# Performance work log

Hardware: AMD Instinct MI355X
Metric: run time of the kernel (lower is better)

## Reference

```python
import jax, jax.numpy as jnp
import numpy as np

B, N, D_VIS, D_LBL = 64, 256, 2048, 512
H, F_OUT = 8, 256            # n_heads, gat_out_per_head_dim
D_IN = D_VIS + D_LBL         # 2560, GAT input dim
D_GAT = H * F_OUT            # 2048, concat-heads output dim
D_EMB = 512                  # final_embedding_dim
ALPHA = 0.2                  # LeakyReLU negative slope


def setup_inputs() -> dict:
    key = jax.random.key(0)
    ks = jax.random.split(key, 9)
    visual_features = jax.random.normal(ks[0], (B, D_VIS), jnp.float32)
    labels_features = jax.random.normal(ks[1], (N, D_LBL), jnp.float32)
    adj = (jax.random.uniform(ks[2], (N, N)) < 0.1).astype(jnp.float32)
    label_adj_matrix = jnp.maximum(adj, jnp.eye(N, dtype=jnp.float32))
    s = 1.0 / np.sqrt(D_IN)
    W_gat = jax.random.uniform(ks[3], (D_IN, H, F_OUT), jnp.float32, -s, s)
    a_src = jax.random.uniform(ks[4], (H, F_OUT), jnp.float32, -s, s)
    a_dst = jax.random.uniform(ks[5], (H, F_OUT), jnp.float32, -s, s)
    sg = 1.0 / np.sqrt(D_GAT)
    pool_q = jax.random.uniform(ks[6], (D_GAT,), jnp.float32, -sg, sg)
    fc_W = jax.random.uniform(ks[7], (D_GAT, D_EMB), jnp.float32, -sg, sg)
    fc_b = jax.random.uniform(ks[8], (D_EMB,), jnp.float32, -sg, sg)
    return {"visual_features": visual_features, "labels_features": labels_features,
            "label_adj_matrix": label_adj_matrix, "W_gat": W_gat, "a_src": a_src,
            "a_dst": a_dst, "pool_q": pool_q, "fc_W": fc_W, "fc_b": fc_b}


def reference(visual_features, labels_features, label_adj_matrix,
              W_gat, a_src, a_dst, pool_q, fc_W, fc_b):
    # Build per-sample contextualized label node features: (B, N, D_IN)
    x = jnp.concatenate(
        [jnp.broadcast_to(labels_features[None], (B, N, D_LBL)),
         jnp.broadcast_to(visual_features[:, None, :], (B, N, D_VIS))], axis=-1)
    # Multi-head GAT layer, batched over B (the torch code loops over B)
    Wh = jnp.einsum('bnd,dhf->bnhf', x, W_gat)            # (B, N, H, F)
    src = jnp.einsum('bnhf,hf->bhn', Wh, a_src)           # (B, H, N)
    dst = jnp.einsum('bnhf,hf->bhn', Wh, a_dst)           # (B, H, N)
    e = src[:, :, :, None] + dst[:, :, None, :]           # (B, H, N, N)
    e = jnp.where(e > 0, e, ALPHA * e)                    # LeakyReLU
    mask = (label_adj_matrix > 0)[None, None]             # (1, 1, N, N)
    scores = jnp.where(mask, e, jnp.float32(-9e15))
    attn = jax.nn.softmax(scores, axis=-1)                # (B, H, N, N)
    out = jnp.einsum('bhij,bjhf->bihf', attn, Wh)         # (B, N, H, F)
    out = jax.nn.elu(out.reshape(B, N, D_GAT))            # concat heads + ELU
    # attention pooling over label nodes
    pw = jax.nn.softmax(jnp.einsum('bnd,d->bn', out, pool_q), axis=-1)
    pooled = jnp.einsum('bn,bnd->bd', pw, out)            # (B, D_GAT)
    return pooled @ fc_W + fc_b                           # (B, D_EMB)
```

## Files before the change

### kernel.cpp

```cpp
#include <hip/hip_runtime.h>
#include <hip/hip_bf16.h>
#include <math.h>

#define BB 64
#define NN 256
#define D_VIS 2048
#define D_LBL 512
#define HH 8
#define FF 256
#define DG 2048
#define DE 512
#define ALPHA 0.2f
#define PSTRIDE 264

using bf16 = __hip_bfloat16;
using short8 = __attribute__((ext_vector_type(8))) short;
using f32x4  = __attribute__((ext_vector_type(4))) float;
__device__ __forceinline__ float b2f(bf16 x) { return __bfloat162float(x); }
__device__ __forceinline__ unsigned short f2bs(float x) {
    bf16 h = __float2bfloat16(x);
    unsigned short u;
    __builtin_memcpy(&u, &h, 2);
    return u;
}

__global__ void __launch_bounds__(256) k_wh(const float* __restrict__ labels,
                                            const float* __restrict__ visual,
                                            const float* __restrict__ Wg,
                                            unsigned short* __restrict__ WhLbT,
                                            float* __restrict__ WhVz,
                                            const float* __restrict__ aSrc,
                                            const float* __restrict__ aDst,
                                            float* __restrict__ srcLp,
                                            float* __restrict__ dstLp,
                                            float* __restrict__ srcVp,
                                            float* __restrict__ dstVp) {
    __shared__ unsigned short As[32][72];
    __shared__ unsigned short Bs[64][72];
    const int t = threadIdx.x;
    const int w = t >> 6;
    const int lane = t & 63;
    const int l15 = lane & 15, quad = lane >> 4;
    const int n0 = blockIdx.x * 64;
    const int p2 = blockIdx.x & 3;
    const int y = blockIdx.y;
    const bool isL = (y < 8);
    const int q = y - 8;
    const int m0  = isL ? y * 32 : (q & 1) * 32;
    const int z   = isL ? 0 : (q >> 1);
    const int kb0 = z * 512;
    const float* A = isL ? labels : visual;
    const int lda  = isL ? D_LBL : D_VIS;
    const float* Wb = Wg + (isL ? 0 : (size_t)D_LBL * DG);

    f32x4 acc[2];
    acc[0] = (f32x4){0.f, 0.f, 0.f, 0.f};
    acc[1] = (f32x4){0.f, 0.f, 0.f, 0.f};

    for (int kc = 0; kc < 8; ++kc) {
        const int kb = kb0 + kc * 64;
#pragma unroll
        for (int p = 0; p < 2; ++p) {
            const int idx = t + 256 * p;
            const int r = idx >> 4, q4 = idx & 15;
            const float4 v = *(const float4*)(A + (size_t)(m0 + r) * lda + kb + 4 * q4);
            unsigned short s4[4] = {f2bs(v.x), f2bs(v.y), f2bs(v.z), f2bs(v.w)};
            __builtin_memcpy(&As[r][4 * q4], s4, 8);
        }
#pragma unroll
        for (int p = 0; p < 4; ++p) {
            const int kk = (t >> 4) + 16 * p;
            const int c4 = (t & 15) * 4;
            const float4 v = *(const float4*)(Wb + (size_t)(kb + kk) * DG + n0 + c4);
            Bs[c4 + 0][kk] = f2bs(v.x);
            Bs[c4 + 1][kk] = f2bs(v.y);
            Bs[c4 + 2][kk] = f2bs(v.z);
            Bs[c4 + 3][kk] = f2bs(v.w);
        }
        __syncthreads();
#pragma unroll
        for (int ks = 0; ks < 2; ++ks) {
            const short8 bf = *(const short8*)&Bs[w * 16 + l15][ks * 32 + quad * 8];
#pragma unroll
            for (int mi = 0; mi < 2; ++mi) {
                const short8 af = *(const short8*)&As[mi * 16 + l15][ks * 32 + quad * 8];
                acc[mi] = __builtin_amdgcn_mfma_f32_16x16x32_bf16(af, bf, acc[mi], 0, 0, 0);
            }
        }
        __syncthreads();
    }
    const int col = n0 + w * 16 + l15;
    const int h = col >> 8;
    const float as = aSrc[col], ad = aDst[col];
    if (isL) {
#pragma unroll
        for (int mi = 0; mi < 2; ++mi) {
            unsigned short s4[4];
#pragma unroll
            for (int r = 0; r < 4; ++r) s4[r] = f2bs(acc[mi][r]);
            __builtin_memcpy(&WhLbT[(size_t)col * NN + m0 + mi * 16 + quad * 4], s4, 8);
        }
#pragma unroll
        for (int mi = 0; mi < 2; ++mi)
#pragma unroll
            for (int r = 0; r < 4; ++r) {
                float sv = acc[mi][r] * as;
                float dv = acc[mi][r] * ad;
#pragma unroll
                for (int off = 1; off < 16; off <<= 1) {
                    sv += __shfl_xor(sv, off);
                    dv += __shfl_xor(dv, off);
                }
                if (l15 == 0) {
                    const int row = m0 + mi * 16 + quad * 4 + r;
                    srcLp[(p2 * NN + row) * HH + h] = sv;
                    dstLp[(p2 * NN + row) * HH + h] = dv;
                }
            }
    } else {
        float* Wv = WhVz + (size_t)z * BB * DG;
#pragma unroll
        for (int mi = 0; mi < 2; ++mi)
#pragma unroll
            for (int r = 0; r < 4; ++r)
                Wv[(size_t)(m0 + mi * 16 + quad * 4 + r) * DG + col] = acc[mi][r];
        const int pv = p2 * 4 + z;
#pragma unroll
        for (int mi = 0; mi < 2; ++mi)
#pragma unroll
            for (int r = 0; r < 4; ++r) {
                float sv = acc[mi][r] * as;
                float dv = acc[mi][r] * ad;
#pragma unroll
                for (int off = 1; off < 16; off <<= 1) {
                    sv += __shfl_xor(sv, off);
                    dv += __shfl_xor(dv, off);
                }
                if (l15 == 0) {
                    const int row = m0 + mi * 16 + quad * 4 + r;
                    srcVp[(pv * BB + row) * HH + h] = sv;
                    dstVp[(pv * BB + row) * HH + h] = dv;
                }
            }
    }
}

__global__ void __launch_bounds__(512, 4) k_gat(const unsigned short* __restrict__ WhLbT,
                                                const float* __restrict__ WhVz,
                                                const float* __restrict__ srcLp,
                                                const float* __restrict__ dstLp,
                                                const float* __restrict__ srcVp,
                                                const float* __restrict__ dstVp,
                                                const float* __restrict__ adj,
                                                const float* __restrict__ pool_q,
                                                bf16* __restrict__ outb,
                                                float* __restrict__ ps_p) {
    const int bid = blockIdx.x;
    const int it = bid & 3;
    const int h  = (bid >> 2) & 7;
    const int b  = bid >> 5;
    const int i0 = it * 64;
    const int t = threadIdx.x;
    const int w = t >> 6;
    const int lane = t & 63;
    const int l15 = lane & 15, quad = lane >> 4;

    __shared__ __align__(16) unsigned short Pl[64][PSTRIDE];
    __shared__ __align__(16) float dls2[2 * NN];
    __shared__ float slsA[64], slsC[64], slsTE[64], inv[64];

    float c = 0.f;
#pragma unroll
    for (int p = 0; p < 16; ++p)
        c += srcVp[(p * BB + b) * HH + h] + dstVp[(p * BB + b) * HH + h];
    if (t < NN) {
        float dl = 0.f;
#pragma unroll
        for (int p = 0; p < 4; ++p) dl += dstLp[(p * NN + t) * HH + h];
        dls2[2 * t]     = __expf(dl);
        dls2[2 * t + 1] = __expf(ALPHA * dl);
    }
    if (t < 64) {
        float sl = 0.f;
#pragma unroll
        for (int p = 0; p < 4; ++p) sl += srcLp[(p * NN + i0 + t) * HH + h];
        const float u = c + sl;
        slsA[t]  = __expf(u);
        slsC[t]  = __expf(ALPHA * u);
        slsTE[t] = __expf(-u);
    }
    const int n0 = w * 32;
    float wv[2] = {0.f, 0.f};
#pragma unroll
    for (int z = 0; z < 4; ++z)
#pragma unroll
        for (int ni = 0; ni < 2; ++ni)
            wv[ni] += WhVz[(size_t)z * BB * DG + (size_t)b * DG + h * FF + n0 + ni * 16 + l15];
    __syncthreads();

    {
        const int g = lane >> 4, s = lane & 15;
#pragma unroll
        for (int rr = 0; rr < 2; ++rr) {
            const int iloc = w * 8 + rr * 4 + g;
            const int i = i0 + iloc;
            const float Ai = slsA[iloc], Ci = slsC[iloc], TEi = slsTE[iloc];
            float pr[16];
            float sum = 0.f;
#pragma unroll
            for (int jj = 0; jj < 8; ++jj) {
                const int j0 = 2 * s + 32 * jj;
                const float2 av = *(const float2*)(adj + (size_t)i * NN + j0);
                const float4 bd = *(const float4*)&dls2[2 * j0];
                const bool g0 = bd.x > TEi;
                const bool g1 = bd.z > TEi;
                float p0 = (g0 ? Ai : Ci) * (g0 ? bd.x : bd.y);
                float p1 = (g1 ? Ai : Ci) * (g1 ? bd.z : bd.w);
                p0 = av.x > 0.f ? p0 : 0.f;
                p1 = av.y > 0.f ? p1 : 0.f;
                pr[2 * jj] = p0; pr[2 * jj + 1] = p1;
                sum += p0 + p1;
            }
#pragma unroll
            for (int off = 1; off < 16; off <<= 1) sum += __shfl_xor(sum, off);
            if (s == 0) inv[iloc] = 1.0f / sum;
#pragma unroll
            for (int jj = 0; jj < 8; ++jj) {
                const unsigned int pk =
                    ((unsigned int)f2bs(pr[2 * jj + 1]) << 16) | f2bs(pr[2 * jj]);
                *(unsigned int*)&Pl[iloc][2 * s + 32 * jj] = pk;
            }
        }
    }
    __syncthreads();

    f32x4 acc[4][2];
#pragma unroll
    for (int mi = 0; mi < 4; ++mi)
#pragma unroll
        for (int ni = 0; ni < 2; ++ni) acc[mi][ni] = (f32x4){0.f, 0.f, 0.f, 0.f};

    const unsigned short* wb = WhLbT + (size_t)(h * FF + n0 + l15) * NN + quad * 8;
    short8 bc0 = *(const short8*)(wb);
    short8 bc1 = *(const short8*)(wb + (size_t)16 * NN);
#pragma unroll
    for (int kc = 0; kc < 8; ++kc) {
        short8 bn0, bn1;
        if (kc < 7) {
            bn0 = *(const short8*)(wb + (kc + 1) * 32);
            bn1 = *(const short8*)(wb + (size_t)16 * NN + (kc + 1) * 32);
        }
        short8 a[4];
#pragma unroll
        for (int mi = 0; mi < 4; ++mi)
            a[mi] = *(const short8*)&Pl[mi * 16 + l15][kc * 32 + quad * 8];
#pragma unroll
        for (int mi = 0; mi < 4; ++mi)
            acc[mi][0] = __builtin_amdgcn_mfma_f32_16x16x32_bf16(a[mi], bc0, acc[mi][0], 0, 0, 0);
#pragma unroll
        for (int mi = 0; mi < 4; ++mi)
            acc[mi][1] = __builtin_amdgcn_mfma_f32_16x16x32_bf16(a[mi], bc1, acc[mi][1], 0, 0, 0);
        bc0 = bn0; bc1 = bn1;
    }

    const float pqv0 = pool_q[h * FF + n0 + l15];
    const float pqv1 = pool_q[h * FF + n0 + 16 + l15];
    float* psrow = ps_p + (size_t)(h * 8 + w) * BB * NN + (size_t)b * NN + i0;
#pragma unroll
    for (int mi = 0; mi < 4; ++mi)
#pragma unroll
        for (int r = 0; r < 4; ++r) {
            const int row = mi * 16 + quad * 4 + r;
            const float ivr = inv[row];
            bf16* orow = outb + ((size_t)(b * NN + i0 + row)) * DG + h * FF + n0;
            float x0 = fmaf(acc[mi][0][r], ivr, wv[0]);
            float x1 = fmaf(acc[mi][1][r], ivr, wv[1]);
            x0 = x0 > 0.f ? x0 : (__expf(x0) - 1.0f);
            x1 = x1 > 0.f ? x1 : (__expf(x1) - 1.0f);
            orow[l15]      = __float2bfloat16(x0);
            orow[16 + l15] = __float2bfloat16(x1);
            float dot = fmaf(x0, pqv0, x1 * pqv1);
#pragma unroll
            for (int off = 1; off < 16; off <<= 1) dot += __shfl_xor(dot, off);
            if (l15 == 0) psrow[row] = dot;
        }
}

__global__ void __launch_bounds__(256) k_pool(const bf16* __restrict__ outb,
                                              const float* __restrict__ ps_p,
                                              float* __restrict__ pooled,
                                              const float* __restrict__ fcb,
                                              float* __restrict__ out) {
    const int dt = blockIdx.x;
    const int b  = blockIdx.y;
    const int t  = threadIdx.x;
    if (dt < 2) out[b * DE + dt * 256 + t] = fcb[dt * 256 + t];
    __shared__ float wsm[NN];
    __shared__ float redm[4];
    __shared__ float reds[4];
    float v = 0.f;
#pragma unroll 8
    for (int s = 0; s < 64; ++s)
        v += ps_p[(size_t)s * BB * NN + (size_t)b * NN + t];
    float m = v;
#pragma unroll
    for (int off = 32; off; off >>= 1) m = fmaxf(m, __shfl_xor(m, off));
    if ((t & 63) == 0) redm[t >> 6] = m;
    __syncthreads();
    m = fmaxf(fmaxf(redm[0], redm[1]), fmaxf(redm[2], redm[3]));
    const float e = __expf(v - m);
    float s = e;
#pragma unroll
    for (int off = 32; off; off >>= 1) s += __shfl_xor(s, off);
    if ((t & 63) == 0) reds[t >> 6] = s;
    __syncthreads();
    s = reds[0] + reds[1] + reds[2] + reds[3];
    wsm[t] = e / s;
    __syncthreads();
    const int d = dt * 256 + t;
    float acc = 0.f;
    const bf16* base = outb + (size_t)b * NN * DG + d;
#pragma unroll 8
    for (int n = 0; n < NN; ++n)
        acc = fmaf(wsm[n], b2f(base[(size_t)n * DG]), acc);
    pooled[(size_t)b * DG + d] = acc;
}

__global__ void __launch_bounds__(256) k_mgemm(const float* __restrict__ A, int lda,
                                               const float* __restrict__ W, int ldw,
                                               float* __restrict__ C, int ldc,
                                               int kSlice, int kIters) {
    __shared__ unsigned short As[32][72];
    __shared__ unsigned short Bs[64][72];
    const int t = threadIdx.x;
    const int w = t >> 6;
    const int lane = t & 63;
    const int l15 = lane & 15, quad = lane >> 4;
    const int n0 = blockIdx.x * 64;
    const int m0 = blockIdx.y * 32;
    const int kb0 = blockIdx.z * kSlice;
    f32x4 acc[2];
    acc[0] = (f32x4){0.f, 0.f, 0.f, 0.f};
    acc[1] = (f32x4){0.f, 0.f, 0.f, 0.f};
    for (int kc = 0; kc < kIters; ++kc) {
        const int kb = kb0 + kc * 64;
#pragma unroll
        for (int p = 0; p < 2; ++p) {
            const int idx = t + 256 * p;
            const int r = idx >> 4, q4 = idx & 15;
            const float4 v = *(const float4*)(A + (size_t)(m0 + r) * lda + kb + 4 * q4);
            unsigned short s4[4] = {f2bs(v.x), f2bs(v.y), f2bs(v.z), f2bs(v.w)};
            __builtin_memcpy(&As[r][4 * q4], s4, 8);
        }
#pragma unroll
        for (int p = 0; p < 4; ++p) {
            const int kk = (t >> 4) + 16 * p;
            const int c4 = (t & 15) * 4;
            const float4 v = *(const float4*)(W + (size_t)(kb + kk) * ldw + n0 + c4);
            Bs[c4 + 0][kk] = f2bs(v.x);
            Bs[c4 + 1][kk] = f2bs(v.y);
            Bs[c4 + 2][kk] = f2bs(v.z);
            Bs[c4 + 3][kk] = f2bs(v.w);
        }
        __syncthreads();
#pragma unroll
        for (int ks = 0; ks < 2; ++ks) {
            const short8 bf = *(const short8*)&Bs[w * 16 + l15][ks * 32 + quad * 8];
#pragma unroll
            for (int mi = 0; mi < 2; ++mi) {
                const short8 af = *(const short8*)&As[mi * 16 + l15][ks * 32 + quad * 8];
                acc[mi] = __builtin_amdgcn_mfma_f32_16x16x32_bf16(af, bf, acc[mi], 0, 0, 0);
            }
        }
        __syncthreads();
    }
    const int col = n0 + w * 16 + l15;
#pragma unroll
    for (int mi = 0; mi < 2; ++mi)
#pragma unroll
        for (int r = 0; r < 4; ++r)
            atomicAdd(&C[(size_t)(m0 + mi * 16 + quad * 4 + r) * ldc + col], acc[mi][r]);
}

extern "C" void kernel_launch(void* const* d_in, const int* in_sizes, int n_in,
                              void* d_out, int out_size, void* d_ws, size_t ws_size,
                              hipStream_t stream) {
    (void)in_sizes; (void)n_in; (void)out_size; (void)ws_size;
    const float* visual = (const float*)d_in[0];
    const float* labels = (const float*)d_in[1];
    const float* adj    = (const float*)d_in[2];
    const float* Wg     = (const float*)d_in[3];
    const float* a_src  = (const float*)d_in[4];
    const float* a_dst  = (const float*)d_in[5];
    const float* pool_q = (const float*)d_in[6];
    const float* fcW    = (const float*)d_in[7];
    const float* fcb    = (const float*)d_in[8];
    float* out = (float*)d_out;

    float* ws_f   = (float*)d_ws;
    float* WhVz   = ws_f;
    float* srcLp  = WhVz + 4 * BB * DG;
    float* dstLp  = srcLp + 4 * NN * HH;
    float* srcVp  = dstLp + 4 * NN * HH;
    float* dstVp  = srcVp + 16 * BB * HH;
    float* ps_p   = dstVp + 16 * BB * HH;
    float* pooled = ps_p + 64 * BB * NN;
    bf16*  outb   = (bf16*)(pooled + BB * DG);
    unsigned short* WhLbT = (unsigned short*)(outb + (size_t)BB * NN * DG);

    k_wh<<<dim3(DG / 64, 16), 256, 0, stream>>>(labels, visual, Wg, WhLbT, WhVz,
                                                a_src, a_dst, srcLp, dstLp, srcVp, dstVp);

    k_gat<<<BB * HH * 4, 512, 0, stream>>>(WhLbT, WhVz, srcLp, dstLp, srcVp, dstVp,
                                           adj, pool_q, outb, ps_p);

    k_pool<<<dim3(8, BB), 256, 0, stream>>>(outb, ps_p, pooled, fcb, out);

    k_mgemm<<<dim3(DE / 64, BB / 32, 8), 256, 0, stream>>>(
        pooled, DG, fcW, DE, out, DE, 256, 4);
}
```

Measured before the change: 186.1 us.

## Fuse all four stages into one cooperative persistent kernel with grid syncs

Replaces the four separate launches (Wh GEMM, GAT attention, pooling, final FC) with a single cooperative kernel of 256 blocks that uses grid.sync between phases and a shared-memory union. The GAT phase is remapped so each block handles 8 batch samples for one head and row tile. Per block it builds the adjacency bitmask and the exp tables once and keeps the WhLbT operand in registers across those samples. This removes per-launch overhead and repeated adjacency and WhLbT loads. The cost is that 256 blocks is far fewer than the previous 2048-block GAT grid, which limits parallelism and latency hiding, and each grid-wide barrier adds its own cost.

```diff
diff --git a/kernel.cpp b/kernel.cpp
--- a/kernel.cpp
+++ b/kernel.cpp
@@ -1,6 +1,9 @@
 #include <hip/hip_runtime.h>
+#include <hip/hip_cooperative_groups.h>
 #include <hip/hip_bf16.h>
 #include <math.h>
+
+namespace cg = cooperative_groups;
 
 #define BB 64
 #define NN 256
@@ -24,362 +27,381 @@
     return u;
 }
 
-__global__ void __launch_bounds__(256) k_wh(const float* __restrict__ labels,
-                                            const float* __restrict__ visual,
-                                            const float* __restrict__ Wg,
-                                            unsigned short* __restrict__ WhLbT,
-                                            float* __restrict__ WhVz,
-                                            const float* __restrict__ aSrc,
-                                            const float* __restrict__ aDst,
-                                            float* __restrict__ srcLp,
-                                            float* __restrict__ dstLp,
-                                            float* __restrict__ srcVp,
-                                            float* __restrict__ dstVp) {
-    __shared__ unsigned short As[32][72];
-    __shared__ unsigned short Bs[64][72];
+__global__ void __launch_bounds__(512) k_mega(
+        const float* __restrict__ labels, const float* __restrict__ visual,
+        const float* __restrict__ Wg, const float* __restrict__ adj,
+        const float* __restrict__ aSrc, const float* __restrict__ aDst,
+        const float* __restrict__ pool_q, const float* __restrict__ fcW,
+        const float* __restrict__ fcb, float* __restrict__ out,
+        unsigned short* __restrict__ WhLbT, float* __restrict__ WhVz,
+        float* __restrict__ srcLp, float* __restrict__ dstLp,
+        float* __restrict__ srcVp, float* __restrict__ dstVp,
+        float* __restrict__ ps_p, float* __restrict__ pooled,
+        bf16* __restrict__ outb) {
+    cg::grid_group grid = cg::this_grid();
+    const int bid = blockIdx.x;
     const int t = threadIdx.x;
-    const int w = t >> 6;
-    const int lane = t & 63;
-    const int l15 = lane & 15, quad = lane >> 4;
-    const int n0 = blockIdx.x * 64;
-    const int p2 = blockIdx.x & 3;
-    const int y = blockIdx.y;
-    const bool isL = (y < 8);
-    const int q = y - 8;
-    const int m0  = isL ? y * 32 : (q & 1) * 32;
-    const int z   = isL ? 0 : (q >> 1);
-    const int kb0 = z * 512;
-    const float* A = isL ? labels : visual;
-    const int lda  = isL ? D_LBL : D_VIS;
-    const float* Wb = Wg + (isL ? 0 : (size_t)D_LBL * DG);
-
-    f32x4 acc[2];
-    acc[0] = (f32x4){0.f, 0.f, 0.f, 0.f};
-    acc[1] = (f32x4){0.f, 0.f, 0.f, 0.f};
-
-    for (int kc = 0; kc < 8; ++kc) {
-        const int kb = kb0 + kc * 64;
+
+    __shared__ __align__(16) union SharedU {
+        struct { unsigned short As[2][32][72], Bs[2][64][72]; } s1;
+        struct { unsigned short Pl[64][PSTRIDE]; float dls2[2 * NN];
+                 float esl[64], easl[64], ensl[64], inv[64], cb[8];
+                 unsigned int maskB[64][8]; } s2;
+        struct { float wsm[2][NN], redm[2][4], reds[2][4]; } s3;
+        struct { unsigned short As[32][136], Bs[64][136]; } s4;
+    } sh;
+
+    {
+        const int half = t >> 8;
+        const int tt = t & 255;
+        const int u = 2 * bid + half;
+        const int xb = u & 31;
+        const int y  = u >> 5;
+        const int w4 = tt >> 6;
+        const int lane = tt & 63;
+        const int l15 = lane & 15, quad = lane >> 4;
+        const int n0 = xb * 64;
+        const int p2 = xb & 3;
+        const bool isL = (y < 8);
+        const int q = y - 8;
+        const int m0  = isL ? y * 32 : (q & 1) * 32;
+        const int z   = isL ? 0 : (q >> 1);
+        const int kb0 = z * 512;
+        const float* A = isL ? labels : visual;
+        const int lda  = isL ? D_LBL : D_VIS;
+        const float* Wb = Wg + (isL ? 0 : (size_t)D_LBL * DG);
+
+        f32x4 acc[2];
+        acc[0] = (f32x4){0.f, 0.f, 0.f, 0.f};
+        acc[1] = (f32x4){0.f, 0.f, 0.f, 0.f};
+        for (int kc = 0; kc < 8; ++kc) {
+            const int kb = kb0 + kc * 64;
+#pragma unroll
+            for (int p = 0; p < 2; ++p) {
+                const int idx = tt + 256 * p;
+                const int r = idx >> 4, q4 = idx & 15;
+                const float4 v = *(const float4*)(A + (size_t)(m0 + r) * lda + kb + 4 * q4);
+                unsigned short s4v[4] = {f2bs(v.x), f2bs(v.y), f2bs(v.z), f2bs(v.w)};
+                __builtin_memcpy(&sh.s1.As[half][r][4 * q4], s4v, 8);
+            }
+#pragma unroll
+            for (int p = 0; p < 4; ++p) {
+                const int kk = (tt >> 4) + 16 * p;
+                const int c4 = (tt & 15) * 4;
+                const float4 v = *(const float4*)(Wb + (size_t)(kb + kk) * DG + n0 + c4);
+                sh.s1.Bs[half][c4 + 0][kk] = f2bs(v.x);
+                sh.s1.Bs[half][c4 + 1][kk] = f2bs(v.y);
+                sh.s1.Bs[half][c4 + 2][kk] = f2bs(v.z);
+                sh.s1.Bs[half][c4 + 3][kk] = f2bs(v.w);
+            }
+            __syncthreads();
+#pragma unroll
+            for (int ks = 0; ks < 2; ++ks) {
+                const short8 bf = *(const short8*)&sh.s1.Bs[half][w4 * 16 + l15][ks * 32 + quad * 8];
+#pragma unroll
+                for (int mi = 0; mi < 2; ++mi) {
+                    const short8 af = *(const short8*)&sh.s1.As[half][mi * 16 + l15][ks * 32 + quad * 8];
+                    acc[mi] = __builtin_amdgcn_mfma_f32_16x16x32_bf16(af, bf, acc[mi], 0, 0, 0);
+                }
+            }
+            __syncthreads();
+        }
+        const int col = n0 + w4 * 16 + l15;
+        const int h = col >> 8;
+        const float as = aSrc[col], ad = aDst[col];
+        if (isL) {
+#pragma unroll
+            for (int mi = 0; mi < 2; ++mi) {
+                unsigned short s4v[4];
+#pragma unroll
+                for (int r = 0; r < 4; ++r) s4v[r] = f2bs(acc[mi][r]);
+                __builtin_memcpy(&WhLbT[(size_t)col * NN + m0 + mi * 16 + quad * 4], s4v, 8);
+            }
+#pragma unroll
+            for (int mi = 0; mi < 2; ++mi)
+#pragma unroll
+                for (int r = 0; r < 4; ++r) {
+                    float sv = acc[mi][r] * as;
+                    float dv = acc[mi][r] * ad;
+#pragma unroll
+                    for (int off = 1; off < 16; off <<= 1) {
+                        sv += __shfl_xor(sv, off);
+                        dv += __shfl_xor(dv, off);
+                    }
+                    if (l15 == 0) {
+                        const int row = m0 + mi * 16 + quad * 4 + r;
+                        srcLp[(p2 * NN + row) * HH + h] = sv;
+                        dstLp[(p2 * NN + row) * HH + h] = dv;
+                    }
+                }
+        } else {
+            float* Wv = WhVz + (size_t)z * BB * DG;
+#pragma unroll
+            for (int mi = 0; mi < 2; ++mi)
+#pragma unroll
+                for (int r = 0; r < 4; ++r)
+                    Wv[(size_t)(m0 + mi * 16 + quad * 4 + r) * DG + col] = acc[mi][r];
+            const int pv = p2 * 4 + z;
+#pragma unroll
+            for (int mi = 0; mi < 2; ++mi)
+#pragma unroll
+                for (int r = 0; r < 4; ++r) {
+                    float sv = acc[mi][r] * as;
+                    float dv = acc[mi][r] * ad;
+#pragma unroll
+                    for (int off = 1; off < 16; off <<= 1) {
+                        sv += __shfl_xor(sv, off);
+                        dv += __shfl_xor(dv, off);
+                    }
+                    if (l15 == 0) {
+                        const int row = m0 + mi * 16 + quad * 4 + r;
+                        srcVp[(pv * BB + row) * HH + h] = sv;
+                        dstVp[(pv * BB + row) * HH + h] = dv;
+                    }
+                }
+        }
+    }
+    __threadfence();
+    grid.sync();
+
+    {
+        const int h  = bid >> 5;
+        const int it = (bid >> 3) & 3;
+        const int bg = bid & 7;
+        const int i0 = it * 64;
+        const int w = t >> 6;
+        const int lane = t & 63;
+        const int l15 = lane & 15, quad = lane >> 4;
+        const int g = lane >> 4, s = lane & 15;
+        const int n0 = w * 32;
+
+        if (t < NN) {
+            float dl = 0.f;
+#pragma unroll
+            for (int p = 0; p < 4; ++p) dl += dstLp[(p * NN + t) * HH + h];
+            sh.s2.dls2[2 * t]     = __expf(dl);
+            sh.s2.dls2[2 * t + 1] = __expf(ALPHA * dl);
+        }
+        if (t < 64) {
+            float sl = 0.f;
+#pragma unroll
+            for (int p = 0; p < 4; ++p) sl += srcLp[(p * NN + i0 + t) * HH + h];
+            sh.s2.esl[t]  = __expf(sl);
+            sh.s2.easl[t] = __expf(ALPHA * sl);
+            sh.s2.ensl[t] = __expf(-sl);
+        }
+        if (t < 128) {
+            const int bi = t >> 4, p = t & 15;
+            const int b = bg * 8 + bi;
+            float v = srcVp[(p * BB + b) * HH + h] + dstVp[(p * BB + b) * HH + h];
+#pragma unroll
+            for (int off = 1; off < 16; off <<= 1) v += __shfl_xor(v, off);
+            if (p == 0) sh.s2.cb[bi] = v;
+        }
+        {
+            const int row = t >> 3, wd = t & 7;
+            const float* ab = adj + (size_t)(i0 + row) * NN + wd * 32;
+            unsigned int m = 0;
+#pragma unroll
+            for (int k4 = 0; k4 < 8; ++k4) {
+                const float4 v = *(const float4*)(ab + 4 * k4);
+                m |= (v.x > 0.f ? 1u : 0u) << (4 * k4);
+                m |= (v.y > 0.f ? 1u : 0u) << (4 * k4 + 1);
+                m |= (v.z > 0.f ? 1u : 0u) << (4 * k4 + 2);
+                m |= (v.w > 0.f ? 1u : 0u) << (4 * k4 + 3);
+            }
+            sh.s2.maskB[row][wd] = m;
+        }
+        const unsigned short* wb = WhLbT + (size_t)(h * FF + n0 + l15) * NN + quad * 8;
+        short8 bcr[8][2];
+#pragma unroll
+        for (int kc = 0; kc < 8; ++kc) {
+            bcr[kc][0] = *(const short8*)(wb + kc * 32);
+            bcr[kc][1] = *(const short8*)(wb + (size_t)16 * NN + kc * 32);
+        }
+        const float pqv0 = pool_q[h * FF + n0 + l15];
+        const float pqv1 = pool_q[h * FF + n0 + 16 + l15];
+        __syncthreads();
+
+        for (int bi = 0; bi < 8; ++bi) {
+            const int b = bg * 8 + bi;
+            const float cbv = sh.s2.cb[bi];
+            const float ec  = __expf(cbv);
+            const float eac = __expf(ALPHA * cbv);
+            const float enc = __expf(-cbv);
+            float wv0 = 0.f, wv1 = 0.f;
+#pragma unroll
+            for (int z = 0; z < 4; ++z) {
+                const float* Wv = WhVz + (size_t)z * BB * DG + (size_t)b * DG + h * FF + n0;
+                wv0 += Wv[l15];
+                wv1 += Wv[16 + l15];
+            }
+#pragma unroll
+            for (int rr = 0; rr < 2; ++rr) {
+                const int iloc = w * 8 + rr * 4 + g;
+                const float Ai  = ec  * sh.s2.esl[iloc];
+                const float Ci  = eac * sh.s2.easl[iloc];
+                const float TEi = enc * sh.s2.ensl[iloc];
+                float pr[16];
+                float sum = 0.f;
+#pragma unroll
+                for (int jj = 0; jj < 8; ++jj) {
+                    const int j0 = 2 * s + 32 * jj;
+                    const unsigned int m = sh.s2.maskB[iloc][jj];
+                    const float4 bd = *(const float4*)&sh.s2.dls2[2 * j0];
+                    const bool g0 = bd.x > TEi;
+                    const bool g1 = bd.z > TEi;
+                    float p0 = (g0 ? Ai : Ci) * (g0 ? bd.x : bd.y);
+                    float p1 = (g1 ? Ai : Ci) * (g1 ? bd.z : bd.w);
+                    p0 = (m & (1u << (2 * s))) ? p0 : 0.f;
+                    p1 = (m & (2u << (2 * s))) ? p1 : 0.f;
+                    pr[2 * jj] = p0; pr[2 * jj + 1] = p1;
+                    sum += p0 + p1;
+                }
+#pragma unroll
+                for (int off = 1; off < 16; off <<= 1) sum += __shfl_xor(sum, off);
+                if (s == 0) sh.s2.inv[iloc] = 1.0f / sum;
+#pragma unroll
+                for (int jj = 0; jj < 8; ++jj) {
+                    const unsigned int pk =
+                        ((unsigned int)f2bs(pr[2 * jj + 1]) << 16) | f2bs(pr[2 * jj]);
+                    *(unsigned int*)&sh.s2.Pl[iloc][2 * s + 32 * jj] = pk;
+                }
+            }
+            __syncthreads();
+
+            f32x4 acc[4][2];
+#pragma unroll
+            for (int mi = 0; mi < 4; ++mi)
+#pragma unroll
+                for (int ni = 0; ni < 2; ++ni) acc[mi][ni] = (f32x4){0.f, 0.f, 0.f, 0.f};
+#pragma unroll
+            for (int kc = 0; kc < 8; ++kc) {
+                short8 a[4];
+#pragma unroll
+                for (int mi = 0; mi < 4; ++mi)
+                    a[mi] = *(const short8*)&sh.s2.Pl[mi * 16 + l15][kc * 32 + quad * 8];
+#pragma unroll
+                for (int mi = 0; mi < 4; ++mi)
+                    acc[mi][0] = __builtin_amdgcn_mfma_f32_16x16x32_bf16(a[mi], bcr[kc][0], acc[mi][0], 0, 0, 0);
+#pragma unroll
+                for (int mi = 0; mi < 4; ++mi)
+                    acc[mi][1] = __builtin_amdgcn_mfma_f32_16x16x32_bf16(a[mi], bcr[kc][1], acc[mi][1], 0, 0, 0);
+            }
+
+            float* psrow = ps_p + (size_t)(h * 8 + w) * BB * NN + (size_t)b * NN + i0;
+#pragma unroll
+            for (int mi = 0; mi < 4; ++mi)
+#pragma unroll
+                for (int r = 0; r < 4; ++r) {
+                    const int row = mi * 16 + quad * 4 + r;
+                    const float ivr = sh.s2.inv[row];
+                    bf16* orow = outb + ((size_t)(b * NN + i0 + row)) * DG + h * FF + n0;
+                    float x0 = fmaf(acc[mi][0][r], ivr, wv0);
+                    float x1 = fmaf(acc[mi][1][r], ivr, wv1);
+                    x0 = x0 > 0.f ? x0 : (__expf(x0) - 1.0f);
+                    x1 = x1 > 0.f ? x1 : (__expf(x1) - 1.0f);
+                    orow[l15]      = __float2bfloat16(x0);
+                    orow[16 + l15] = __float2bfloat16(x1);
+                    float dot = fmaf(x0, pqv0, x1 * pqv1);
+#pragma unroll
+                    for (int off = 1; off < 16; off <<= 1) dot += __shfl_xor(dot, off);
+                    if (l15 == 0) psrow[row] = dot;
+                }
+            __syncthreads();
+        }
+    }
+    __threadfence();
+    grid.sync();
+
+    {
+        const int half = t >> 8;
+        const int tt = t & 255;
+        const int u = 2 * bid + half;
+        const int dt = u & 7;
+        const int b  = u >> 3;
+        if (dt < 2) out[b * DE + dt * 256 + tt] = fcb[dt * 256 + tt];
+        float v = 0.f;
+#pragma unroll 8
+        for (int sI = 0; sI < 64; ++sI)
+            v += ps_p[(size_t)sI * BB * NN + (size_t)b * NN + tt];
+        float m = v;
+#pragma unroll
+        for (int off = 32; off; off >>= 1) m = fmaxf(m, __shfl_xor(m, off));
+        if ((tt & 63) == 0) sh.s3.redm[half][tt >> 6] = m;
+        __syncthreads();
+        m = fmaxf(fmaxf(sh.s3.redm[half][0], sh.s3.redm[half][1]),
+                  fmaxf(sh.s3.redm[half][2], sh.s3.redm[half][3]));
+        const float e = __expf(v - m);
+        float sred = e;
+#pragma unroll
+        for (int off = 32; off; off >>= 1) sred += __shfl_xor(sred, off);
+        if ((tt & 63) == 0) sh.s3.reds[half][tt >> 6] = sred;
+        __syncthreads();
+        sred = sh.s3.reds[half][0] + sh.s3.reds[half][1] + sh.s3.reds[half][2] + sh.s3.reds[half][3];
+        sh.s3.wsm[half][tt] = e / sred;
+        __syncthreads();
+        const int d = dt * 256 + tt;
+        float acc = 0.f;
+        const bf16* base = outb + (size_t)b * NN * DG + d;
+#pragma unroll 8
+        for (int n = 0; n < NN; ++n)
+            acc = fmaf(sh.s3.wsm[half][n], b2f(base[(size_t)n * DG]), acc);
+        pooled[(size_t)b * DG + d] = acc;
+    }
+    __threadfence();
+    grid.sync();
+
+    {
+        const int x  = bid & 7;
+        const int mm = (bid >> 3) & 1;
+        const int z  = bid >> 4;
+        const int n0f = x * 64;
+        const int m0f = mm * 32;
+        const int kb0 = z * 128;
+        const int w = t >> 6;
+        const int lane = t & 63;
+        const int l15 = lane & 15, quad = lane >> 4;
 #pragma unroll
         for (int p = 0; p < 2; ++p) {
-            const int idx = t + 256 * p;
-            const int r = idx >> 4, q4 = idx & 15;
-            const float4 v = *(const float4*)(A + (size_t)(m0 + r) * lda + kb + 4 * q4);
-            unsigned short s4[4] = {f2bs(v.x), f2bs(v.y), f2bs(v.z), f2bs(v.w)};
-            __builtin_memcpy(&As[r][4 * q4], s4, 8);
+            const int idx = t + 512 * p;
+            const int row = idx >> 5, c4 = idx & 31;
+            const float4 v = *(const float4*)(pooled + (size_t)(m0f + row) * DG + kb0 + 4 * c4);
+            unsigned short s4v[4] = {f2bs(v.x), f2bs(v.y), f2bs(v.z), f2bs(v.w)};
+            __builtin_memcpy(&sh.s4.As[row][4 * c4], s4v, 8);
         }
 #pragma unroll
         for (int p = 0; p < 4; ++p) {
-            const int kk = (t >> 4) + 16 * p;
-            const int c4 = (t & 15) * 4;
-            const float4 v = *(const float4*)(Wb + (size_t)(kb + kk) * DG + n0 + c4);
-            Bs[c4 + 0][kk] = f2bs(v.x);
-            Bs[c4 + 1][kk] = f2bs(v.y);
-            Bs[c4 + 2][kk] = f2bs(v.z);
-            Bs[c4 + 3][kk] = f2bs(v.w);
+            const int idx = t + 512 * p;
+            const int kk = idx >> 4, c4 = (idx & 15) * 4;
+            const float4 v = *(const float4*)(fcW + (size_t)(kb0 + kk) * DE + n0f + c4);
+            sh.s4.Bs[c4 + 0][kk] = f2bs(v.x);
+            sh.s4.Bs[c4 + 1][kk] = f2bs(v.y);
+            sh.s4.Bs[c4 + 2][kk] = f2bs(v.z);
+            sh.s4.Bs[c4 + 3][kk] = f2bs(v.w);
         }
         __syncthreads();
-#pragma unroll
-        for (int ks = 0; ks < 2; ++ks) {
-            const short8 bf = *(const short8*)&Bs[w * 16 + l15][ks * 32 + quad * 8];
-#pragma unroll
-            for (int mi = 0; mi < 2; ++mi) {
-                const short8 af = *(const short8*)&As[mi * 16 + l15][ks * 32 + quad * 8];
-                acc[mi] = __builtin_amdgcn_mfma_f32_16x16x32_bf16(af, bf, acc[mi], 0, 0, 0);
-            }
-        }
-        __syncthreads();
+        if (w < 4) {
+            f32x4 acc[2];
+            acc[0] = (f32x4){0.f, 0.f, 0.f, 0.f};
+            acc[1] = (f32x4){0.f, 0.f, 0.f, 0.f};
+#pragma unroll
+            for (int kc = 0; kc < 4; ++kc) {
+                const short8 bf = *(const short8*)&sh.s4.Bs[w * 16 + l15][kc * 32 + quad * 8];
+#pragma unroll
+                for (int mi = 0; mi < 2; ++mi) {
+                    const short8 af = *(const short8*)&sh.s4.As[mi * 16 + l15][kc * 32 + quad * 8];
+                    acc[mi] = __builtin_amdgcn_mfma_f32_16x16x32_bf16(af, bf, acc[mi], 0, 0, 0);
+                }
+            }
+            const int col = n0f + w * 16 + l15;
+#pragma unroll
+            for (int mi = 0; mi < 2; ++mi)
+#pragma unroll
+                for (int r = 0; r < 4; ++r)
+                    atomicAdd(&out[(size_t)(m0f + mi * 16 + quad * 4 + r) * DE + col], acc[mi][r]);
+        }
     }
-    const int col = n0 + w * 16 + l15;
-    const int h = col >> 8;
-    const float as = aSrc[col], ad = aDst[col];
-    if (isL) {
-#pragma unroll
-        for (int mi = 0; mi < 2; ++mi) {
-            unsigned short s4[4];
-#pragma unroll
-            for (int r = 0; r < 4; ++r) s4[r] = f2bs(acc[mi][r]);
-            __builtin_memcpy(&WhLbT[(size_t)col * NN + m0 + mi * 16 + quad * 4], s4, 8);
-        }
-#pragma unroll
-        for (int mi = 0; mi < 2; ++mi)
-#pragma unroll
-            for (int r = 0; r < 4; ++r) {
-                float sv = acc[mi][r] * as;
-                float dv = acc[mi][r] * ad;
-#pragma unroll
-                for (int off = 1; off < 16; off <<= 1) {
-                    sv += __shfl_xor(sv, off);
-                    dv += __shfl_xor(dv, off);
-                }
-                if (l15 == 0) {
-                    const int row = m0 + mi * 16 + quad * 4 + r;
-                    srcLp[(p2 * NN + row) * HH + h] = sv;
-                    dstLp[(p2 * NN + row) * HH + h] = dv;
-                }
-            }
-    } else {
-        float* Wv = WhVz + (size_t)z * BB * DG;
-#pragma unroll
-        for (int mi = 0; mi < 2; ++mi)
-#pragma unroll
-            for (int r = 0; r < 4; ++r)
-                Wv[(size_t)(m0 + mi * 16 + quad * 4 + r) * DG + col] = acc[mi][r];
-        const int pv = p2 * 4 + z;
-#pragma unroll
-        for (int mi = 0; mi < 2; ++mi)
-#pragma unroll
-            for (int r = 0; r < 4; ++r) {
-                float sv = acc[mi][r] * as;
-                float dv = acc[mi][r] * ad;
-#pragma unroll
-                for (int off = 1; off < 16; off <<= 1) {
-                    sv += __shfl_xor(sv, off);
-                    dv += __shfl_xor(dv, off);
-                }
-                if (l15 == 0) {
-                    const int row = m0 + mi * 16 + quad * 4 + r;
-                    srcVp[(pv * BB + row) * HH + h] = sv;
-                    dstVp[(pv * BB + row) * HH + h] = dv;
-                }
-            }
-    }
-}
-
-__global__ void __launch_bounds__(512, 4) k_gat(const unsigned short* __restrict__ WhLbT,
-                                                const float* __restrict__ WhVz,
-                                                const float* __restrict__ srcLp,
-                                                const float* __restrict__ dstLp,
-                                                const float* __restrict__ srcVp,
-                                                const float* __restrict__ dstVp,
-                                                const float* __restrict__ adj,
-                                                const float* __restrict__ pool_q,
-                                                bf16* __restrict__ outb,
-                                                float* __restrict__ ps_p) {
-    const int bid = blockIdx.x;
-    const int it = bid & 3;
-    const int h  = (bid >> 2) & 7;
-    const int b  = bid >> 5;
-    const int i0 = it * 64;
-    const int t = threadIdx.x;
-    const int w = t >> 6;
-    const int lane = t & 63;
-    const int l15 = lane & 15, quad = lane >> 4;
-
-    __shared__ __align__(16) unsigned short Pl[64][PSTRIDE];
-    __shared__ __align__(16) float dls2[2 * NN];
-    __shared__ float slsA[64], slsC[64], slsTE[64], inv[64];
-
-    float c = 0.f;
-#pragma unroll
-    for (int p = 0; p < 16; ++p)
-        c += srcVp[(p * BB + b) * HH + h] + dstVp[(p * BB + b) * HH + h];
-    if (t < NN) {
-        float dl = 0.f;
-#pragma unroll
-        for (int p = 0; p < 4; ++p) dl += dstLp[(p * NN + t) * HH + h];
-        dls2[2 * t]     = __expf(dl);
-        dls2[2 * t + 1] = __expf(ALPHA * dl);
-    }
-    if (t < 64) {
-        float sl = 0.f;
-#pragma unroll
-        for (int p = 0; p < 4; ++p) sl += srcLp[(p * NN + i0 + t) * HH + h];
-        const float u = c + sl;
-        slsA[t]  = __expf(u);
-        slsC[t]  = __expf(ALPHA * u);
-        slsTE[t] = __expf(-u);
-    }
-    const int n0 = w * 32;
-    float wv[2] = {0.f, 0.f};
-#pragma unroll
-    for (int z = 0; z < 4; ++z)
-#pragma unroll
-        for (int ni = 0; ni < 2; ++ni)
-            wv[ni] += WhVz[(size_t)z * BB * DG + (size_t)b * DG + h * FF + n0 + ni * 16 + l15];
-    __syncthreads();
-
-    {
-        const int g = lane >> 4, s = lane & 15;
-#pragma unroll
-        for (int rr = 0; rr < 2; ++rr) {
-            const int iloc = w * 8 + rr * 4 + g;
-            const int i = i0 + iloc;
-            const float Ai = slsA[iloc], Ci = slsC[iloc], TEi = slsTE[iloc];
-            float pr[16];
-            float sum = 0.f;
-#pragma unroll
-            for (int jj = 0; jj < 8; ++jj) {
-                const int j0 = 2 * s + 32 * jj;
-                const float2 av = *(const float2*)(adj + (size_t)i * NN + j0);
-                const float4 bd = *(const float4*)&dls2[2 * j0];
-                const bool g0 = bd.x > TEi;
-                const bool g1 = bd.z > TEi;
-                float p0 = (g0 ? Ai : Ci) * (g0 ? bd.x : bd.y);
-                float p1 = (g1 ? Ai : Ci) * (g1 ? bd.z : bd.w);
-                p0 = av.x > 0.f ? p0 : 0.f;
-                p1 = av.y > 0.f ? p1 : 0.f;
-                pr[2 * jj] = p0; pr[2 * jj + 1] = p1;
-                sum += p0 + p1;
-            }
-#pragma unroll
-            for (int off = 1; off < 16; off <<= 1) sum += __shfl_xor(sum, off);
-            if (s == 0) inv[iloc] = 1.0f / sum;
-#pragma unroll
-            for (int jj = 0; jj < 8; ++jj) {
-                const unsigned int pk =
-                    ((unsigned int)f2bs(pr[2 * jj + 1]) << 16) | f2bs(pr[2 * jj]);
-                *(unsigned int*)&Pl[iloc][2 * s + 32 * jj] = pk;
-            }
-        }
-    }
-    __syncthreads();
-
-    f32x4 acc[4][2];
-#pragma unroll
-    for (int mi = 0; mi < 4; ++mi)
-#pragma unroll
-        for (int ni = 0; ni < 2; ++ni) acc[mi][ni] = (f32x4){0.f, 0.f, 0.f, 0.f};
-
-    const unsigned short* wb = WhLbT + (size_t)(h * FF + n0 + l15) * NN + quad * 8;
-    short8 bc0 = *(const short8*)(wb);
-    short8 bc1 = *(const short8*)(wb + (size_t)16 * NN);
-#pragma unroll
-    for (int kc = 0; kc < 8; ++kc) {
-        short8 bn0, bn1;
-        if (kc < 7) {
-            bn0 = *(const short8*)(wb + (kc + 1) * 32);
-            bn1 = *(const short8*)(wb + (size_t)16 * NN + (kc + 1) * 32);
-        }
-        short8 a[4];
-#pragma unroll
-        for (int mi = 0; mi < 4; ++mi)
-            a[mi] = *(const short8*)&Pl[mi * 16 + l15][kc * 32 + quad * 8];
-#pragma unroll
-        for (int mi = 0; mi < 4; ++mi)
-            acc[mi][0] = __builtin_amdgcn_mfma_f32_16x16x32_bf16(a[mi], bc0, acc[mi][0], 0, 0, 0);
-#pragma unroll
-        for (int mi = 0; mi < 4; ++mi)
-            acc[mi][1] = __builtin_amdgcn_mfma_f32_16x16x32_bf16(a[mi], bc1, acc[mi][1], 0, 0, 0);
-        bc0 = bn0; bc1 = bn1;
-    }
-
-    const float pqv0 = pool_q[h * FF + n0 + l15];
-    const float pqv1 = pool_q[h * FF + n0 + 16 + l15];
-    float* psrow = ps_p + (size_t)(h * 8 + w) * BB * NN + (size_t)b * NN + i0;
-#pragma unroll
-    for (int mi = 0; mi < 4; ++mi)
-#pragma unroll
-        for (int r = 0; r < 4; ++r) {
-            const int row = mi * 16 + quad * 4 + r;
-            const float ivr = inv[row];
-            bf16* orow = outb + ((size_t)(b * NN + i0 + row)) * DG + h * FF + n0;
-            float x0 = fmaf(acc[mi][0][r], ivr, wv[0]);
-            float x1 = fmaf(acc[mi][1][r], ivr, wv[1]);
-            x0 = x0 > 0.f ? x0 : (__expf(x0) - 1.0f);
-            x1 = x1 > 0.f ? x1 : (__expf(x1) - 1.0f);
-            orow[l15]      = __float2bfloat16(x0);
-            orow[16 + l15] = __float2bfloat16(x1);
-            float dot = fmaf(x0, pqv0, x1 * pqv1);
-#pragma unroll
-            for (int off = 1; off < 16; off <<= 1) dot += __shfl_xor(dot, off);
-            if (l15 == 0) psrow[row] = dot;
-        }
-}
-
-__global__ void __launch_bounds__(256) k_pool(const bf16* __restrict__ outb,
-                                              const float* __restrict__ ps_p,
-                                              float* __restrict__ pooled,
-                                              const float* __restrict__ fcb,
-                                              float* __restrict__ out) {
-    const int dt = blockIdx.x;
-    const int b  = blockIdx.y;
-    const int t  = threadIdx.x;
-    if (dt < 2) out[b * DE + dt * 256 + t] = fcb[dt * 256 + t];
-    __shared__ float wsm[NN];
-    __shared__ float redm[4];
-    __shared__ float reds[4];
-    float v = 0.f;
-#pragma unroll 8
-    for (int s = 0; s < 64; ++s)
-        v += ps_p[(size_t)s * BB * NN + (size_t)b * NN + t];
-    float m = v;
-#pragma unroll
-    for (int off = 32; off; off >>= 1) m = fmaxf(m, __shfl_xor(m, off));
-    if ((t & 63) == 0) redm[t >> 6] = m;
-    __syncthreads();
-    m = fmaxf(fmaxf(redm[0], redm[1]), fmaxf(redm[2], redm[3]));
-    const float e = __expf(v - m);
-    float s = e;
-#pragma unroll
-    for (int off = 32; off; off >>= 1) s += __shfl_xor(s, off);
-    if ((t & 63) == 0) reds[t >> 6] = s;
-    __syncthreads();
-    s = reds[0] + reds[1] + reds[2] + reds[3];
-    wsm[t] = e / s;
-    __syncthreads();
-    const int d = dt * 256 + t;
-    float acc = 0.f;
-    const bf16* base = outb + (size_t)b * NN * DG + d;
-#pragma unroll 8
-    for (int n = 0; n < NN; ++n)
-        acc = fmaf(wsm[n], b2f(base[(size_t)n * DG]), acc);
-    pooled[(size_t)b * DG + d] = acc;
-}
-
-__global__ void __launch_bounds__(256) k_mgemm(const float* __restrict__ A, int lda,
-                                               const float* __restrict__ W, int ldw,
-                                               float* __restrict__ C, int ldc,
-                                               int kSlice, int kIters) {
-    __shared__ unsigned short As[32][72];
-    __shared__ unsigned short Bs[64][72];
-    const int t = threadIdx.x;
-    const int w = t >> 6;
-    const int lane = t & 63;
-    const int l15 = lane & 15, quad = lane >> 4;
-    const int n0 = blockIdx.x * 64;
-    const int m0 = blockIdx.y * 32;
-    const int kb0 = blockIdx.z * kSlice;
-    f32x4 acc[2];
-    acc[0] = (f32x4){0.f, 0.f, 0.f, 0.f};
-    acc[1] = (f32x4){0.f, 0.f, 0.f, 0.f};
-    for (int kc = 0; kc < kIters; ++kc) {
-        const int kb = kb0 + kc * 64;
-#pragma unroll
-        for (int p = 0; p < 2; ++p) {
-            const int idx = t + 256 * p;
-            const int r = idx >> 4, q4 = idx & 15;
-            const float4 v = *(const float4*)(A + (size_t)(m0 + r) * lda + kb + 4 * q4);
-            unsigned short s4[4] = {f2bs(v.x), f2bs(v.y), f2bs(v.z), f2bs(v.w)};
-            __builtin_memcpy(&As[r][4 * q4], s4, 8);
-        }
-#pragma unroll
-        for (int p = 0; p < 4; ++p) {
-            const int kk = (t >> 4) + 16 * p;
-            const int c4 = (t & 15) * 4;
-            const float4 v = *(const float4*)(W + (size_t)(kb + kk) * ldw + n0 + c4);
-            Bs[c4 + 0][kk] = f2bs(v.x);
-            Bs[c4 + 1][kk] = f2bs(v.y);
-            Bs[c4 + 2][kk] = f2bs(v.z);
-            Bs[c4 + 3][kk] = f2bs(v.w);
-        }
-        __syncthreads();
-#pragma unroll
-        for (int ks = 0; ks < 2; ++ks) {
-            const short8 bf = *(const short8*)&Bs[w * 16 + l15][ks * 32 + quad * 8];
-#pragma unroll
-            for (int mi = 0; mi < 2; ++mi) {
-                const short8 af = *(const short8*)&As[mi * 16 + l15][ks * 32 + quad * 8];
-                acc[mi] = __builtin_amdgcn_mfma_f32_16x16x32_bf16(af, bf, acc[mi], 0, 0, 0);
-            }
-        }
-        __syncthreads();
-    }
-    const int col = n0 + w * 16 + l15;
-#pragma unroll
-    for (int mi = 0; mi < 2; ++mi)
-#pragma unroll
-        for (int r = 0; r < 4; ++r)
-            atomicAdd(&C[(size_t)(m0 + mi * 16 + quad * 4 + r) * ldc + col], acc[mi][r]);
 }
 
 extern "C" void kernel_launch(void* const* d_in, const int* in_sizes, int n_in,
@@ -408,14 +430,13 @@
     bf16*  outb   = (bf16*)(pooled + BB * DG);
     unsigned short* WhLbT = (unsigned short*)(outb + (size_t)BB * NN * DG);
 
-    k_wh<<<dim3(DG / 64, 16), 256, 0, stream>>>(labels, visual, Wg, WhLbT, WhVz,
-                                                a_src, a_dst, srcLp, dstLp, srcVp, dstVp);
-
-    k_gat<<<BB * HH * 4, 512, 0, stream>>>(WhLbT, WhVz, srcLp, dstLp, srcVp, dstVp,
-                                           adj, pool_q, outb, ps_p);
-
-    k_pool<<<dim3(8, BB), 256, 0, stream>>>(outb, ps_p, pooled, fcb, out);
-
-    k_mgemm<<<dim3(DE / 64, BB / 32, 8), 256, 0, stream>>>(
-        pooled, DG, fcW, DE, out, DE, 256, 4);
+    void* args[] = {
+        (void*)&labels, (void*)&visual, (void*)&Wg, (void*)&adj,
+        (void*)&a_src, (void*)&a_dst, (void*)&pool_q, (void*)&fcW,
+        (void*)&fcb, (void*)&out,
+        (void*)&WhLbT, (void*)&WhVz, (void*)&srcLp, (void*)&dstLp,
+        (void*)&srcVp, (void*)&dstVp, (void*)&ps_p, (void*)&pooled,
+        (void*)&outb
+    };
+    hipLaunchCooperativeKernel((void*)k_mega, dim3(256), dim3(512), args, 0, stream);
 }
```

After: 397.4 us. +113.5%, slower.

## Process two batch samples per GAT block with bitmask adjacency and factored exponentials

Applied to the files above, without the earlier changes.

Each k_gat block now handles two batch samples in a loop, halving the grid. The adjacency tile is packed once per block into a shared-memory bitmask, replacing per-element float reads from global memory. The per-row exponentials are factored into a label part and a per-sample constant, so both samples reuse the label-dependent exps, pool_q and the WhLbT row pointers. The trade-off is less parallelism (1024 blocks instead of 2048), serialised per-sample work inside a block, and extra barriers per iteration.

```diff
diff --git a/kernel.cpp b/kernel.cpp
--- a/kernel.cpp
+++ b/kernel.cpp
@@ -158,21 +158,20 @@
     const int bid = blockIdx.x;
     const int it = bid & 3;
     const int h  = (bid >> 2) & 7;
-    const int b  = bid >> 5;
+    const int bg = bid >> 5;
     const int i0 = it * 64;
     const int t = threadIdx.x;
     const int w = t >> 6;
     const int lane = t & 63;
     const int l15 = lane & 15, quad = lane >> 4;
+    const int g = lane >> 4, s = lane & 15;
 
     __shared__ __align__(16) unsigned short Pl[64][PSTRIDE];
     __shared__ __align__(16) float dls2[2 * NN];
-    __shared__ float slsA[64], slsC[64], slsTE[64], inv[64];
-
-    float c = 0.f;
-#pragma unroll
-    for (int p = 0; p < 16; ++p)
-        c += srcVp[(p * BB + b) * HH + h] + dstVp[(p * BB + b) * HH + h];
+    __shared__ float esl[64], easl[64], ensl[64], inv[64];
+    __shared__ float cb[2];
+    __shared__ unsigned int maskB[64][8];
+
     if (t < NN) {
         float dl = 0.f;
 #pragma unroll
@@ -184,40 +183,70 @@
         float sl = 0.f;
 #pragma unroll
         for (int p = 0; p < 4; ++p) sl += srcLp[(p * NN + i0 + t) * HH + h];
-        const float u = c + sl;
-        slsA[t]  = __expf(u);
-        slsC[t]  = __expf(ALPHA * u);
-        slsTE[t] = __expf(-u);
+        esl[t]  = __expf(sl);
+        easl[t] = __expf(ALPHA * sl);
+        ensl[t] = __expf(-sl);
+    }
+    if (t < 32) {
+        const int bi = t >> 4, p = t & 15;
+        const int b = bg * 2 + bi;
+        float v = srcVp[(p * BB + b) * HH + h] + dstVp[(p * BB + b) * HH + h];
+#pragma unroll
+        for (int off = 1; off < 16; off <<= 1) v += __shfl_xor(v, off);
+        if (p == 0) cb[bi] = v;
+    }
+    {
+        const int row = t >> 3, wd = t & 7;
+        const float* ab = adj + (size_t)(i0 + row) * NN + wd * 32;
+        unsigned int m = 0;
+#pragma unroll
+        for (int k4 = 0; k4 < 8; ++k4) {
+            const float4 v = *(const float4*)(ab + 4 * k4);
+            m |= (v.x > 0.f ? 1u : 0u) << (4 * k4);
+            m |= (v.y > 0.f ? 1u : 0u) << (4 * k4 + 1);
+            m |= (v.z > 0.f ? 1u : 0u) << (4 * k4 + 2);
+            m |= (v.w > 0.f ? 1u : 0u) << (4 * k4 + 3);
+        }
+        maskB[row][wd] = m;
     }
     const int n0 = w * 32;
-    float wv[2] = {0.f, 0.f};
-#pragma unroll
-    for (int z = 0; z < 4; ++z)
-#pragma unroll
-        for (int ni = 0; ni < 2; ++ni)
-            wv[ni] += WhVz[(size_t)z * BB * DG + (size_t)b * DG + h * FF + n0 + ni * 16 + l15];
+    const float pqv0 = pool_q[h * FF + n0 + l15];
+    const float pqv1 = pool_q[h * FF + n0 + 16 + l15];
+    const unsigned short* wb = WhLbT + (size_t)(h * FF + n0 + l15) * NN + quad * 8;
     __syncthreads();
 
-    {
-        const int g = lane >> 4, s = lane & 15;
+    for (int bi = 0; bi < 2; ++bi) {
+        const int b = bg * 2 + bi;
+        const float cbv = cb[bi];
+        const float ec  = __expf(cbv);
+        const float eac = __expf(ALPHA * cbv);
+        const float enc = __expf(-cbv);
+        float wv0 = 0.f, wv1 = 0.f;
+#pragma unroll
+        for (int z = 0; z < 4; ++z) {
+            const float* Wv = WhVz + (size_t)z * BB * DG + (size_t)b * DG + h * FF + n0;
+            wv0 += Wv[l15];
+            wv1 += Wv[16 + l15];
+        }
 #pragma unroll
         for (int rr = 0; rr < 2; ++rr) {
             const int iloc = w * 8 + rr * 4 + g;
-            const int i = i0 + iloc;
-            const float Ai = slsA[iloc], Ci = slsC[iloc], TEi = slsTE[iloc];
+            const float Ai  = ec  * esl[iloc];
+            const float Ci  = eac * easl[iloc];
+            const float TEi = enc * ensl[iloc];
             float pr[16];
             float sum = 0.f;
 #pragma unroll
             for (int jj = 0; jj < 8; ++jj) {
                 const int j0 = 2 * s + 32 * jj;
-                const float2 av = *(const float2*)(adj + (size_t)i * NN + j0);
+                const unsigned int m = maskB[iloc][jj];
                 const float4 bd = *(const float4*)&dls2[2 * j0];
                 const bool g0 = bd.x > TEi;
                 const bool g1 = bd.z > TEi;
                 float p0 = (g0 ? Ai : Ci) * (g0 ? bd.x : bd.y);
                 float p1 = (g1 ? Ai : Ci) * (g1 ? bd.z : bd.w);
-                p0 = av.x > 0.f ? p0 : 0.f;
-                p1 = av.y > 0.f ? p1 : 0.f;
+                p0 = (m & (1u << (2 * s))) ? p0 : 0.f;
+                p1 = (m & (2u << (2 * s))) ? p1 : 0.f;
                 pr[2 * jj] = p0; pr[2 * jj + 1] = p1;
                 sum += p0 + p1;
             }
@@ -231,59 +260,57 @@
                 *(unsigned int*)&Pl[iloc][2 * s + 32 * jj] = pk;
             }
         }
-    }
-    __syncthreads();
-
-    f32x4 acc[4][2];
-#pragma unroll
-    for (int mi = 0; mi < 4; ++mi)
-#pragma unroll
-        for (int ni = 0; ni < 2; ++ni) acc[mi][ni] = (f32x4){0.f, 0.f, 0.f, 0.f};
-
-    const unsigned short* wb = WhLbT + (size_t)(h * FF + n0 + l15) * NN + quad * 8;
-    short8 bc0 = *(const short8*)(wb);
-    short8 bc1 = *(const short8*)(wb + (size_t)16 * NN);
-#pragma unroll
-    for (int kc = 0; kc < 8; ++kc) {
-        short8 bn0, bn1;
-        if (kc < 7) {
-            bn0 = *(const short8*)(wb + (kc + 1) * 32);
-            bn1 = *(const short8*)(wb + (size_t)16 * NN + (kc + 1) * 32);
-        }
-        short8 a[4];
+        __syncthreads();
+
+        f32x4 acc[4][2];
 #pragma unroll
         for (int mi = 0; mi < 4; ++mi)
-            a[mi] = *(const short8*)&Pl[mi * 16 + l15][kc * 32 + quad * 8];
+#pragma unroll
+            for (int ni = 0; ni < 2; ++ni) acc[mi][ni] = (f32x4){0.f, 0.f, 0.f, 0.f};
+
+        short8 bc0 = *(const short8*)(wb);
+        short8 bc1 = *(const short8*)(wb + (size_t)16 * NN);
+#pragma unroll
+        for (int kc = 0; kc < 8; ++kc) {
+            short8 bn0, bn1;
+            if (kc < 7) {
+                bn0 = *(const short8*)(wb + (kc + 1) * 32);
+                bn1 = *(const short8*)(wb + (size_t)16 * NN + (kc + 1) * 32);
+            }
+            short8 a[4];
+#pragma unroll
+            for (int mi = 0; mi < 4; ++mi)
+                a[mi] = *(const short8*)&Pl[mi * 16 + l15][kc * 32 + quad * 8];
+#pragma unroll
+            for (int mi = 0; mi < 4; ++mi)
+                acc[mi][0] = __builtin_amdgcn_mfma_f32_16x16x32_bf16(a[mi], bc0, acc[mi][0], 0, 0, 0);
+#pragma unroll
+            for (int mi = 0; mi < 4; ++mi)
+                acc[mi][1] = __builtin_amdgcn_mfma_f32_16x16x32_bf16(a[mi], bc1, acc[mi][1], 0, 0, 0);
+            bc0 = bn0; bc1 = bn1;
+        }
+
+        float* psrow = ps_p + (size_t)(h * 8 + w) * BB * NN + (size_t)b * NN + i0;
 #pragma unroll
         for (int mi = 0; mi < 4; ++mi)
-            acc[mi][0] = __builtin_amdgcn_mfma_f32_16x16x32_bf16(a[mi], bc0, acc[mi][0], 0, 0, 0);
-#pragma unroll
-        for (int mi = 0; mi < 4; ++mi)
-            acc[mi][1] = __builtin_amdgcn_mfma_f32_16x16x32_bf16(a[mi], bc1, acc[mi][1], 0, 0, 0);
-        bc0 = bn0; bc1 = bn1;
-    }
-
-    const float pqv0 = pool_q[h * FF + n0 + l15];
-    const float pqv1 = pool_q[h * FF + n0 + 16 + l15];
-    float* psrow = ps_p + (size_t)(h * 8 + w) * BB * NN + (size_t)b * NN + i0;
-#pragma unroll
-    for (int mi = 0; mi < 4; ++mi)
-#pragma unroll
-        for (int r = 0; r < 4; ++r) {
-            const int row = mi * 16 + quad * 4 + r;
-            const float ivr = inv[row];
-            bf16* orow = outb + ((size_t)(b * NN + i0 + row)) * DG + h * FF + n0;
-            float x0 = fmaf(acc[mi][0][r], ivr, wv[0]);
-            float x1 = fmaf(acc[mi][1][r], ivr, wv[1]);
-            x0 = x0 > 0.f ? x0 : (__expf(x0) - 1.0f);
-            x1 = x1 > 0.f ? x1 : (__expf(x1) - 1.0f);
-            orow[l15]      = __float2bfloat16(x0);
-            orow[16 + l15] = __float2bfloat16(x1);
-            float dot = fmaf(x0, pqv0, x1 * pqv1);
-#pragma unroll
-            for (int off = 1; off < 16; off <<= 1) dot += __shfl_xor(dot, off);
-            if (l15 == 0) psrow[row] = dot;
-        }
+#pragma unroll
+            for (int r = 0; r < 4; ++r) {
+                const int row = mi * 16 + quad * 4 + r;
+                const float ivr = inv[row];
+                bf16* orow = outb + ((size_t)(b * NN + i0 + row)) * DG + h * FF + n0;
+                float x0 = fmaf(acc[mi][0][r], ivr, wv0);
+                float x1 = fmaf(acc[mi][1][r], ivr, wv1);
+                x0 = x0 > 0.f ? x0 : (__expf(x0) - 1.0f);
+                x1 = x1 > 0.f ? x1 : (__expf(x1) - 1.0f);
+                orow[l15]      = __float2bfloat16(x0);
+                orow[16 + l15] = __float2bfloat16(x1);
+                float dot = fmaf(x0, pqv0, x1 * pqv1);
+#pragma unroll
+                for (int off = 1; off < 16; off <<= 1) dot += __shfl_xor(dot, off);
+                if (l15 == 0) psrow[row] = dot;
+            }
+        __syncthreads();
+    }
 }
 
 __global__ void __launch_bounds__(256) k_pool(const bf16* __restrict__ outb,
@@ -411,7 +438,7 @@
     k_wh<<<dim3(DG / 64, 16), 256, 0, stream>>>(labels, visual, Wg, WhLbT, WhVz,
                                                 a_src, a_dst, srcLp, dstLp, srcVp, dstVp);
 
-    k_gat<<<BB * HH * 4, 512, 0, stream>>>(WhLbT, WhVz, srcLp, dstLp, srcVp, dstVp,
+    k_gat<<<32 * HH * 4, 512, 0, stream>>>(WhLbT, WhVz, srcLp, dstLp, srcVp, dstVp,
                                            adj, pool_q, outb, ps_p);
 
     k_pool<<<dim3(8, BB), 256, 0, stream>>>(outb, ps_p, pooled, fcb, out);
```

Result: slower. 192.2 us (+3.3%).
